# Kernel optimization log

Measured on AMD Instinct MI355X. Metric: run time of the kernel, lower is better.

Reference implementation:

```python
import jax, jax.numpy as jnp
import numpy as np

NUM_USERS = 100000
NUM_ITEMS = 50000
N_NODES = NUM_USERS + NUM_ITEMS
EMBED_DIM = 64
N_EDGES = 2400000
NUM_LAYERS = 3
DROPOUT_P = 0.2


def setup_inputs() -> dict:
    key = jax.random.key(0)
    k1, k2, k3, k4, k5 = jax.random.split(key, 5)
    # xavier_uniform bound = sqrt(6/(fan_in+fan_out))
    bu = np.sqrt(6.0 / (NUM_USERS + EMBED_DIM)).astype(np.float32)
    bi = np.sqrt(6.0 / (NUM_ITEMS + EMBED_DIM)).astype(np.float32)
    user_emb = jax.random.uniform(k1, (NUM_USERS, EMBED_DIM), jnp.float32, -bu, bu)
    item_emb = jax.random.uniform(k2, (NUM_ITEMS, EMBED_DIM), jnp.float32, -bi, bi)
    adj_rows = jax.random.randint(k3, (N_EDGES,), 0, N_NODES, dtype=jnp.int32)
    adj_cols = jax.random.randint(k4, (N_EDGES,), 0, N_NODES, dtype=jnp.int32)
    # normalized adjacency values (positive, small) mimicking D^-1/2 A D^-1/2
    adj_vals = jax.random.uniform(k5, (N_EDGES,), jnp.float32, 0.0, 0.25)
    return {"user_emb": user_emb, "item_emb": item_emb,
            "adj_rows": adj_rows, "adj_cols": adj_cols, "adj_vals": adj_vals}


def _spmm(rows, cols, vals, x):
    # y[r] += vals[e] * x[cols[e]] for each edge e with rows[e]==r
    gathered = x[cols] * vals[:, None]          # [E, D]
    return jax.ops.segment_sum(gathered, rows, num_segments=N_NODES)


def reference(user_emb, item_emb, adj_rows, adj_cols, adj_vals):
    x = jnp.concatenate([user_emb, item_emb], axis=0)          # [N, D]
    # dropout (training=True), fixed key for determinism
    keep = jax.random.bernoulli(jax.random.key(42), 1.0 - DROPOUT_P, x.shape)
    x = jnp.where(keep, x / (1.0 - DROPOUT_P), 0.0)
    acc = x  # running sum over layer embeddings (== mean * (L+1))
    for _ in range(NUM_LAYERS):
        x = _spmm(adj_rows, adj_cols, adj_vals, x)
        acc = acc + x
    final = acc / jnp.float32(NUM_LAYERS + 1)
    return final[:NUM_USERS], final[NUM_USERS:]
```

## Files before the change

kernel.cpp:

```cpp
#include <hip/hip_runtime.h>


static constexpr int NU = 100000;
static constexpr int NI = 50000;
static constexpr int NN = NU + NI;
static constexpr int D  = 64;
static constexpr int E  = 2400000;
static constexpr int XN = NN * D;
static constexpr int XH = XN / 2;
static constexpr int NB = (NN + 1023) >> 10;
static constexpr int BPC = 24000;
static constexpr int BIN_T = 256;
static constexpr int BIN_U = 16;
static constexpr int BIN_CHUNK = BIN_T * BIN_U;

typedef _Float16 half_t;
typedef _Float16 half8 __attribute__((ext_vector_type(8)));

__device__ __forceinline__ unsigned rotl32(unsigned x, int r) {
    return (x << r) | (x >> (32 - r));
}

__device__ __forceinline__ void threefry2x32(unsigned k0, unsigned k1,
                                             unsigned x0, unsigned x1,
                                             unsigned& o0, unsigned& o1) {
    unsigned ks2 = k0 ^ k1 ^ 0x1BD11BDAu;
    x0 += k0; x1 += k1;
#define TF_R(r) { x0 += x1; x1 = rotl32(x1, r); x1 ^= x0; }
    TF_R(13) TF_R(15) TF_R(26) TF_R(6)   x0 += k1;  x1 += ks2 + 1u;
    TF_R(17) TF_R(29) TF_R(16) TF_R(24)  x0 += ks2; x1 += k0 + 2u;
    TF_R(13) TF_R(15) TF_R(26) TF_R(6)   x0 += k0;  x1 += k1 + 3u;
    TF_R(17) TF_R(29) TF_R(16) TF_R(24)  x0 += k1;  x1 += ks2 + 4u;
    TF_R(13) TF_R(15) TF_R(26) TF_R(6)   x0 += ks2; x1 += k0 + 5u;
#undef TF_R
    o0 = x0; o1 = x1;
}

__device__ __forceinline__ float dropout_val(const float* __restrict__ ue,
                                             const float* __restrict__ ie,
                                             int i, unsigned bits) {
    float src = (i < NU * D) ? ue[i] : ie[i - NU * D];
    float u = __uint_as_float((bits >> 9) | 0x3f800000u) - 1.0f;
    return (u < 0.8f) ? (src / 0.8f) : 0.0f;
}

__global__ void k_dropout_init(const float* __restrict__ ue,
                               const float* __restrict__ ie,
                               half_t* __restrict__ x0h) {
    int j = blockIdx.x * blockDim.x + threadIdx.x;
    if (j >= XH) return;
    unsigned o0, o1, b0, b1;
    threefry2x32(0u, 42u, 0u, (unsigned)j, o0, o1);        b0 = o0 ^ o1;
    threefry2x32(0u, 42u, 0u, (unsigned)(j + XH), o0, o1); b1 = o0 ^ o1;
    x0h[j]      = (half_t)dropout_val(ue, ie, j, b0);
    x0h[j + XH] = (half_t)dropout_val(ue, ie, j + XH, b1);
}

__global__ void __launch_bounds__(BIN_T) k_bin(const int* __restrict__ rows,
                                               const int* __restrict__ cols,
                                               const float* __restrict__ vals,
                                               int2* __restrict__ stg,
                                               int* __restrict__ pcnt) {
    __shared__ int lcnt[NB];
    __shared__ int gbase[NB];
    int tid = threadIdx.x;
    for (int i = tid; i < NB; i += BIN_T) lcnt[i] = 0;
    __syncthreads();
    int base = blockIdx.x * BIN_CHUNK;
    int lp[BIN_U];
    int2 rec[BIN_U];
    #pragma unroll
    for (int u = 0; u < BIN_U; ++u) {
        int idx = base + u * BIN_T + tid;
        if (idx < E) {
            int row = rows[idx];
            int col = cols[idx];
            float v = vals[idx];
            unsigned q = min(__float2int_rn(v * 65536.f), 16383);
            int b = row >> 10;
            int loff = atomicAdd(&lcnt[b], 1);
            lp[u] = (b << 13) | loff;
            rec[u] = make_int2((int)((q << 18) | (unsigned)col), row);
        } else {
            lp[u] = -1;
        }
    }
    __syncthreads();
    for (int i = tid; i < NB; i += BIN_T)
        gbase[i] = atomicAdd(&pcnt[i * 16], lcnt[i]);
    __syncthreads();
    #pragma unroll
    for (int u = 0; u < BIN_U; ++u) {
        if (lp[u] >= 0) {
            int b = lp[u] >> 13;
            int pos = gbase[b] + (lp[u] & 8191);
            if (pos < BPC) stg[(size_t)b * BPC + pos] = rec[u];
        }
    }
}

__global__ void k_bscan(const int* __restrict__ pcnt, int* __restrict__ bbase,
                        int* __restrict__ rp) {
    int lane = threadIdx.x;
    int carry = 0;
    for (int base = 0; base < NB; base += 64) {
        int i = base + lane;
        int v = (i < NB) ? pcnt[i * 16] : 0;
        int x = v;
        #pragma unroll
        for (int d = 1; d < 64; d <<= 1) {
            int y = __shfl_up(x, d);
            if (lane >= d) x += y;
        }
        if (i < NB) bbase[i] = carry + x - v;
        carry += __shfl(x, 63);
    }
    if (lane == 0) rp[NN] = E;
}

__global__ void __launch_bounds__(1024) k_bsort(const int2* __restrict__ stg,
                                                const int* __restrict__ pcnt,
                                                const int* __restrict__ bbase,
                                                int* __restrict__ rp,
                                                unsigned* __restrict__ ev) {
    __shared__ int cnt[1024];
    __shared__ int wsum[16];
    int b = blockIdx.x;
    int t = threadIdx.x;
    cnt[t] = 0;
    __syncthreads();
    int tot = min(pcnt[b * 16], BPC);
    int bb = bbase[b];
    const int2* s = stg + (size_t)b * BPC;
    for (int i = t; i < tot; i += 1024)
        atomicAdd(&cnt[s[i].y & 1023], 1);
    __syncthreads();
    int v = cnt[t];
    int lane = t & 63, w = t >> 6;
    int x = v;
    #pragma unroll
    for (int d = 1; d < 64; d <<= 1) {
        int y = __shfl_up(x, d);
        if (lane >= d) x += y;
    }
    if (lane == 63) wsum[w] = x;
    __syncthreads();
    if (w == 0 && lane < 16) {
        int sv = wsum[lane];
        #pragma unroll
        for (int d = 1; d < 16; d <<= 1) {
            int y = __shfl_up(sv, d);
            if (lane >= d) sv += y;
        }
        wsum[lane] = sv;
    }
    __syncthreads();
    int excl = ((w > 0) ? wsum[w - 1] : 0) + x - v;
    int row = (b << 10) + t;
    if (row < NN) rp[row] = bb + excl;
    __syncthreads();
    cnt[t] = bb + excl;
    __syncthreads();
    for (int i = t; i < tot; i += 1024) {
        int2 r = s[i];
        int pos = atomicAdd(&cnt[r.y & 1023], 1);
        ev[pos] = (unsigned)r.x;
    }
}

template <int MODE>
__global__ void __launch_bounds__(256) k_spmm(const int* __restrict__ rp,
                                              const unsigned* __restrict__ ev,
                                              const half_t* __restrict__ xh,
                                              half_t* __restrict__ yh,
                                              const half_t* __restrict__ x0h,
                                              const half_t* __restrict__ y1h,
                                              float* __restrict__ out) {
    int row = blockIdx.x * 4 + (threadIdx.x >> 6);
    if (row >= NN) return;
    int lane = threadIdx.x & 63;
    int grp = lane >> 3;
    int sl  = lane & 7;
    const float inv = 1.0f / 65536.0f;
    int s0 = rp[row];
    int cnt = rp[row + 1] - s0;
    float acc[8] = {0.f, 0.f, 0.f, 0.f, 0.f, 0.f, 0.f, 0.f};
    for (int base = 0; base < cnt; base += 64) {
        int idx = base + lane;
        int pc = (idx < cnt) ? (int)ev[s0 + idx] : 0;
        int m = min(64, cnt - base);
        int mm = (m + 15) & ~15;
        for (int jj = 0; jj < mm; jj += 16) {
            int pj0 = __shfl(pc, jj + grp);
            int pj1 = __shfl(pc, jj + 8 + grp);
            int   c0 = pj0 & 0x3FFFF;
            float v0 = (float)((unsigned)pj0 >> 18) * inv;
            int   c1 = pj1 & 0x3FFFF;
            float v1 = (float)((unsigned)pj1 >> 18) * inv;
            const half8 xa = *(const half8*)(xh + c0 * 64 + sl * 8);
            const half8 xb = *(const half8*)(xh + c1 * 64 + sl * 8);
            #pragma unroll
            for (int k = 0; k < 8; ++k) acc[k] = fmaf(v0, (float)xa[k], acc[k]);
            #pragma unroll
            for (int k = 0; k < 8; ++k) acc[k] = fmaf(v1, (float)xb[k], acc[k]);
        }
    }
    #pragma unroll
    for (int mask = 8; mask <= 32; mask <<= 1) {
        #pragma unroll
        for (int k = 0; k < 8; ++k) acc[k] += __shfl_xor(acc[k], mask);
    }
    if (grp == 0) {
        int o = row * 64 + sl * 8;
        if (MODE == 0) {
            half8 st;
            #pragma unroll
            for (int k = 0; k < 8; ++k) st[k] = (half_t)acc[k];
            *(half8*)(yh + o) = st;
        } else {
            const half8 a0 = *(const half8*)(x0h + o);
            const half8 a1 = *(const half8*)(y1h + o);
            const half8 a2 = *(const half8*)(xh + o);
            float r[8];
            #pragma unroll
            for (int k = 0; k < 8; ++k)
                r[k] = ((float)a0[k] + (float)a1[k] + (float)a2[k] + acc[k]) * 0.25f;
            *(float4*)(out + o)     = make_float4(r[0], r[1], r[2], r[3]);
            *(float4*)(out + o + 4) = make_float4(r[4], r[5], r[6], r[7]);
        }
    }
}

extern "C" void kernel_launch(void* const* d_in, const int* in_sizes, int n_in,
                              void* d_out, int out_size, void* d_ws, size_t ws_size,
                              hipStream_t stream) {
    const float* ue   = (const float*)d_in[0];
    const float* ie   = (const float*)d_in[1];
    const int*   rows = (const int*)d_in[2];
    const int*   cols = (const int*)d_in[3];
    const float* vals = (const float*)d_in[4];
    float* out = (float*)d_out;

    half_t*   X0h   = (half_t*)d_ws;
    half_t*   Y1h   = X0h + XN;
    half_t*   Y2h   = Y1h + XN;
    int2*     stg   = (int2*)Y1h;
    unsigned* ev    = (unsigned*)(Y2h + XN);
    int*      rp    = (int*)(ev + E);
    int*      pcnt  = rp + NN + 4;
    int*      bbase = pcnt + NB * 16;

    (void)hipMemsetAsync(pcnt, 0, (NB * 16 + NB) * sizeof(int), stream);
    k_dropout_init<<<(XH + 255) / 256, 256, 0, stream>>>(ue, ie, X0h);
    k_bin<<<(E + BIN_CHUNK - 1) / BIN_CHUNK, BIN_T, 0, stream>>>(rows, cols, vals, stg, pcnt);
    k_bscan<<<1, 64, 0, stream>>>(pcnt, bbase, rp);
    k_bsort<<<NB, 1024, 0, stream>>>(stg, pcnt, bbase, rp, ev);

    int sgrid = (NN + 3) / 4;
    k_spmm<0><<<sgrid, 256, 0, stream>>>(rp, ev, X0h, Y1h, nullptr, nullptr, nullptr);
    k_spmm<0><<<sgrid, 256, 0, stream>>>(rp, ev, Y1h, Y2h, nullptr, nullptr, nullptr);
    k_spmm<1><<<sgrid, 256, 0, stream>>>(rp, ev, Y2h, nullptr, X0h, Y1h, out);
}
```

Before: 343.1 us.

## Map one 8-lane group per row in SpMM instead of one wavefront per row

The SpMM kernel now assigns each row to an 8-lane subgroup, so a wavefront handles 8 rows at once, instead of spreading one row's edges across all 64 lanes. This drops the cross-lane shuffle-xor reduction and the idle lanes seen with rows of only ~16 edges on average. It also cuts the padded work when a row's edge count is not a multiple of 16. In exchange, lanes within a wave diverge when row lengths differ, and each subgroup walks its edges serially in chunks of 8.

```diff
diff --git a/kernel.cpp b/kernel.cpp
--- a/kernel.cpp
+++ b/kernel.cpp
@@ -176,58 +176,52 @@
                                               const half_t* __restrict__ x0h,
                                               const half_t* __restrict__ y1h,
                                               float* __restrict__ out) {
-    int row = blockIdx.x * 4 + (threadIdx.x >> 6);
+    int wid  = threadIdx.x >> 6;
+    int lane = threadIdx.x & 63;
+    int g    = lane >> 3;
+    int l    = lane & 7;
+    int row  = blockIdx.x * 32 + wid * 8 + g;
     if (row >= NN) return;
-    int lane = threadIdx.x & 63;
-    int grp = lane >> 3;
-    int sl  = lane & 7;
     const float inv = 1.0f / 65536.0f;
-    int s0 = rp[row];
+    int s0  = rp[row];
     int cnt = rp[row + 1] - s0;
     float acc[8] = {0.f, 0.f, 0.f, 0.f, 0.f, 0.f, 0.f, 0.f};
-    for (int base = 0; base < cnt; base += 64) {
-        int idx = base + lane;
+    int gl = g << 3;
+    for (int base = 0; base < cnt; base += 8) {
+        int idx = base + l;
         int pc = (idx < cnt) ? (int)ev[s0 + idx] : 0;
-        int m = min(64, cnt - base);
-        int mm = (m + 15) & ~15;
-        for (int jj = 0; jj < mm; jj += 16) {
-            int pj0 = __shfl(pc, jj + grp);
-            int pj1 = __shfl(pc, jj + 8 + grp);
-            int   c0 = pj0 & 0x3FFFF;
-            float v0 = (float)((unsigned)pj0 >> 18) * inv;
-            int   c1 = pj1 & 0x3FFFF;
-            float v1 = (float)((unsigned)pj1 >> 18) * inv;
-            const half8 xa = *(const half8*)(xh + c0 * 64 + sl * 8);
-            const half8 xb = *(const half8*)(xh + c1 * 64 + sl * 8);
+        #pragma unroll
+        for (int j = 0; j < 8; j += 2) {
+            int p0 = __shfl(pc, gl | j);
+            int p1 = __shfl(pc, gl | (j + 1));
+            int   c0 = p0 & 0x3FFFF;
+            float v0 = (float)((unsigned)p0 >> 18) * inv;
+            int   c1 = p1 & 0x3FFFF;
+            float v1 = (float)((unsigned)p1 >> 18) * inv;
+            const half8 xa = *(const half8*)(xh + c0 * 64 + l * 8);
+            const half8 xb = *(const half8*)(xh + c1 * 64 + l * 8);
             #pragma unroll
             for (int k = 0; k < 8; ++k) acc[k] = fmaf(v0, (float)xa[k], acc[k]);
             #pragma unroll
             for (int k = 0; k < 8; ++k) acc[k] = fmaf(v1, (float)xb[k], acc[k]);
         }
     }
-    #pragma unroll
-    for (int mask = 8; mask <= 32; mask <<= 1) {
-        #pragma unroll
-        for (int k = 0; k < 8; ++k) acc[k] += __shfl_xor(acc[k], mask);
-    }
-    if (grp == 0) {
-        int o = row * 64 + sl * 8;
-        if (MODE == 0) {
-            half8 st;
-            #pragma unroll
-            for (int k = 0; k < 8; ++k) st[k] = (half_t)acc[k];
-            *(half8*)(yh + o) = st;
-        } else {
-            const half8 a0 = *(const half8*)(x0h + o);
-            const half8 a1 = *(const half8*)(y1h + o);
-            const half8 a2 = *(const half8*)(xh + o);
-            float r[8];
-            #pragma unroll
-            for (int k = 0; k < 8; ++k)
-                r[k] = ((float)a0[k] + (float)a1[k] + (float)a2[k] + acc[k]) * 0.25f;
-            *(float4*)(out + o)     = make_float4(r[0], r[1], r[2], r[3]);
-            *(float4*)(out + o + 4) = make_float4(r[4], r[5], r[6], r[7]);
-        }
+    int o = row * 64 + l * 8;
+    if (MODE == 0) {
+        half8 st;
+        #pragma unroll
+        for (int k = 0; k < 8; ++k) st[k] = (half_t)acc[k];
+        *(half8*)(yh + o) = st;
+    } else {
+        const half8 a0 = *(const half8*)(x0h + o);
+        const half8 a1 = *(const half8*)(y1h + o);
+        const half8 a2 = *(const half8*)(xh + o);
+        float r[8];
+        #pragma unroll
+        for (int k = 0; k < 8; ++k)
+            r[k] = ((float)a0[k] + (float)a1[k] + (float)a2[k] + acc[k]) * 0.25f;
+        *(float4*)(out + o)     = make_float4(r[0], r[1], r[2], r[3]);
+        *(float4*)(out + o + 4) = make_float4(r[4], r[5], r[6], r[7]);
     }
 }
 
@@ -256,7 +250,7 @@
     k_bscan<<<1, 64, 0, stream>>>(pcnt, bbase, rp);
     k_bsort<<<NB, 1024, 0, stream>>>(stg, pcnt, bbase, rp, ev);
 
-    int sgrid = (NN + 3) / 4;
+    int sgrid = (NN + 31) / 32;
     k_spmm<0><<<sgrid, 256, 0, stream>>>(rp, ev, X0h, Y1h, nullptr, nullptr, nullptr);
     k_spmm<0><<<sgrid, 256, 0, stream>>>(rp, ev, Y1h, Y2h, nullptr, nullptr, nullptr);
     k_spmm<1><<<sgrid, 256, 0, stream>>>(rp, ev, Y2h, nullptr, X0h, Y1h, out);
```

Result: faster. 318.6 us (-7.1%).
